# Performance work log

Hardware: AMD Instinct MI355X
Metric: run time of the kernel (lower is better)

Reference implementation:

```python
import jax, jax.numpy as jnp
import numpy as np

B, C, H, W = 8, 64, 256, 256
M1, M2 = 16, 16  # half of n_modes=(32,32); rfft last dim keeps n_modes[-1]//2


def setup_inputs() -> dict:
    key = jax.random.key(0)
    ks = jax.random.split(key, 7)
    scale = 1.0 / (C * C)
    return {
        "x": jax.random.normal(ks[0], (B, C, H, W), dtype=jnp.float32),
        "w1r": scale * jax.random.normal(ks[1], (C, C, M1, M2), dtype=jnp.float32),
        "w1i": scale * jax.random.normal(ks[2], (C, C, M1, M2), dtype=jnp.float32),
        "w2r": scale * jax.random.normal(ks[3], (C, C, M1, M2), dtype=jnp.float32),
        "w2i": scale * jax.random.normal(ks[4], (C, C, M1, M2), dtype=jnp.float32),
        "conv_w": jax.random.normal(ks[5], (C, C), dtype=jnp.float32) / np.sqrt(C),
        "conv_b": jax.random.normal(ks[6], (C,), dtype=jnp.float32) * 0.01,
    }


def reference(x, w1r, w1i, w2r, w2i, conv_w, conv_b):
    # ---- SpectralConv branch ----
    # rfft2 over spatial dims with 'ortho' norm: [b, c, H, W//2+1] complex
    x_ft = jnp.fft.rfftn(x, axes=(2, 3), norm="ortho")
    w1 = w1r + 1j * w1i  # positive-frequency corner weights [i, o, m1, m2]
    w2 = w2r + 1j * w2i  # negative-frequency corner weights
    top = jnp.einsum("bixy,ioxy->boxy", x_ft[:, :, :M1, :M2], w1)
    bot = jnp.einsum("bixy,ioxy->boxy", x_ft[:, :, -M1:, :M2], w2)
    out_ft = jnp.zeros((B, C, H, W // 2 + 1), dtype=x_ft.dtype)
    out_ft = out_ft.at[:, :, :M1, :M2].set(top)
    out_ft = out_ft.at[:, :, -M1:, :M2].set(bot)
    x1 = jnp.fft.irfftn(out_ft, s=(H, W), axes=(2, 3), norm="ortho")
    # ---- 1x1 Conv1d residual branch (channel mixing) ----
    x2 = jnp.einsum("oi,bixy->boxy", conv_w, x) + conv_b[None, :, None, None]
    return x1 + x2
```

## Files before the change

### kernel.cpp

```cpp
#include <hip/hip_runtime.h>
#include <math.h>


#define TWOPI_256 0.024543692606170259f
#define INV256    0.00390625f

#define NX   262144
#define NWT  2097152
#define NZ   2097152
#define O_TA  0
#define O_TB  4096
#define O_XR  20480
#define O_XI  (O_XR + NX)
#define O_WTR (O_XI + NX)
#define O_WTI (O_WTR + NWT)
#define O_YR  (O_WTI + NWT)
#define O_YI  (O_YR + NX)
#define O_ZR  (O_YI + NX)
#define O_ZI  (O_ZR + NZ)
#define O_TT  (O_ZI + NZ)
#define O_TD  (O_TT + 4096)

using s16x8 = __attribute__((ext_vector_type(8))) short;
using f32x4 = __attribute__((ext_vector_type(4))) float;

__device__ __forceinline__ unsigned short f2bf(float f) {
    union { float f; unsigned u; } a; a.f = f;
    unsigned r = (a.u + 0x7fffu + ((a.u >> 16) & 1u)) >> 16;
    return (unsigned short)r;
}

__global__ __launch_bounds__(256) void ktabs(unsigned short* __restrict__ tA,
                                             unsigned short* __restrict__ tB,
                                             unsigned short* __restrict__ tD) {
    int idx = blockIdx.x * 256 + threadIdx.x;
    if (idx < 8192) {
        int col = idx >> 8, w = idx & 255;
        int ky = col & 15;
        int mm = (ky * w) & 255;
        float s, c; sincosf((float)mm * TWOPI_256, &s, &c);
        tA[idx] = f2bf(col < 16 ? c * INV256 : -s * INV256);
    } else if (idx < 40960) {
        int j = idx - 8192;
        int kx2 = j >> 9, k = j & 511, h = k >> 1, p = k & 1;
        int kxi = kx2 & 31;
        int kx = (kxi < 16) ? kxi : (224 + kxi);
        int mm = (kx * h) & 255;
        float s, c; sincosf((float)mm * TWOPI_256, &s, &c);
        float v;
        if (kx2 < 32) v = p ? s : c;
        else          v = p ? c : -s;
        tB[j] = f2bf(v);
    } else {
        int j = idx - 40960;
        int ri = j >> 14, rem = j & 16383;
        int h = rem >> 6, k = rem & 63, kxi = k >> 1, p = k & 1;
        int kx = (kxi < 16) ? kxi : (224 + kxi);
        int mm = (kx * h) & 255;
        float s, c; sincosf((float)mm * TWOPI_256, &s, &c);
        float v;
        if (ri == 0) v = p ? -s : c;
        else         v = p ? c : s;
        tD[j] = f2bf(v);
    }
}

__global__ __launch_bounds__(256) void kab_fwd(const float* __restrict__ x,
                                               const unsigned short* __restrict__ tA,
                                               const unsigned short* __restrict__ tB,
                                               float* __restrict__ Xr,
                                               float* __restrict__ Xi) {
    __shared__ __align__(16) unsigned short xt[16384];
    __shared__ __align__(16) unsigned int   ub[4096];
    const int tid  = threadIdx.x;
    const int bc   = blockIdx.x;
    const int m    = tid & 15;
    const int g    = (tid >> 4) & 3;
    const int wave = tid >> 6;

    const float* xp = x + (size_t)bc * 65536;

    f32x4 acc[2][4];
#pragma unroll
    for (int a = 0; a < 2; ++a)
#pragma unroll
        for (int fn = 0; fn < 4; ++fn)
#pragma unroll
            for (int r = 0; r < 4; ++r) acc[a][fn][r] = 0.f;

    for (int ch = 0; ch < 4; ++ch) {
#pragma unroll
        for (int it = 0; it < 16; ++it) {
            int h  = it * 16 + (tid >> 4);
            int w4 = tid & 15;
            float4 v = *reinterpret_cast<const float4*>(xp + h * 256 + ch * 64 + w4 * 4);
            unsigned lo = (unsigned)f2bf(v.x) | ((unsigned)f2bf(v.y) << 16);
            unsigned hi = (unsigned)f2bf(v.z) | ((unsigned)f2bf(v.w) << 16);
            int wl  = w4 * 4;
            int blk = (wl >> 3) ^ (h & 7);
            char* p = reinterpret_cast<char*>(xt) + (h << 7) + (blk << 4) + ((wl & 7) << 1);
            *reinterpret_cast<uint2*>(p) = make_uint2(lo, hi);
        }
        __syncthreads();
#pragma unroll
        for (int ks = 0; ks < 2; ++ks) {
            s16x8 a0 = *reinterpret_cast<const s16x8*>(tA + m * 256        + ch * 64 + ks * 32 + 8 * g);
            s16x8 a1 = *reinterpret_cast<const s16x8*>(tA + (16 + m) * 256 + ch * 64 + ks * 32 + 8 * g);
#pragma unroll
            for (int fn = 0; fn < 4; ++fn) {
                int h   = wave * 64 + fn * 16 + m;
                int blk = (4 * ks + g) ^ (h & 7);
                s16x8 bf = *reinterpret_cast<const s16x8*>(
                    reinterpret_cast<const char*>(xt) + (h << 7) + (blk << 4));
                acc[0][fn] = __builtin_amdgcn_mfma_f32_16x16x32_bf16(a0, bf, acc[0][fn], 0, 0, 0);
                acc[1][fn] = __builtin_amdgcn_mfma_f32_16x16x32_bf16(a1, bf, acc[1][fn], 0, 0, 0);
            }
        }
        __syncthreads();
    }

#pragma unroll
    for (int fn = 0; fn < 4; ++fn) {
        int h = wave * 64 + fn * 16 + m;
#pragma unroll
        for (int r = 0; r < 4; ++r) {
            int ky = 4 * g + r;
            unsigned pk = (unsigned)f2bf(acc[0][fn][r]) | ((unsigned)f2bf(acc[1][fn][r]) << 16);
            int blk = (h >> 2) ^ (ky & 7);
            ub[ky * 256 + blk * 4 + (h & 3)] = pk;
        }
    }
    __syncthreads();

    f32x4 acc2;
#pragma unroll
    for (int r = 0; r < 4; ++r) acc2[r] = 0.f;
#pragma unroll
    for (int ks = 0; ks < 16; ++ks) {
        s16x8 a2 = *reinterpret_cast<const s16x8*>(tB + (wave * 16 + m) * 512 + ks * 32 + 8 * g);
        int blk = (4 * ks + g) ^ (m & 7);
        s16x8 b2 = *reinterpret_cast<const s16x8*>(
            reinterpret_cast<const char*>(ub) + m * 1024 + (blk << 4));
        acc2 = __builtin_amdgcn_mfma_f32_16x16x32_bf16(a2, b2, acc2, 0, 0, 0);
    }
#pragma unroll
    for (int r = 0; r < 4; ++r) {
        int kx2 = wave * 16 + 4 * g + r;
        if (kx2 < 32) Xr[(size_t)bc * 512 + kx2 * 16 + m]        = acc2[r];
        else          Xi[(size_t)bc * 512 + (kx2 - 32) * 16 + m] = acc2[r];
    }
}

__global__ __launch_bounds__(256) void kw_prep(const float* __restrict__ w1r,
                                               const float* __restrict__ w1i,
                                               const float* __restrict__ w2r,
                                               const float* __restrict__ w2i,
                                               float* __restrict__ Wtr,
                                               float* __restrict__ Wti) {
    __shared__ float lds[128][65];
    const int tid = threadIdx.x;
    const int a = blockIdx.x >> 6;
    const int i = blockIdx.x & 63;
    const float* src = (a == 0) ? w1r : (a == 1) ? w1i : (a == 2) ? w2r : w2i;
    float* dst = (a & 1) ? Wti : Wtr;
    const int kxoff = (a >> 1) << 4;
    const float* sp = src + (size_t)i * 16384;

    for (int p = 0; p < 2; ++p) {
        if (p) __syncthreads();
#pragma unroll
        for (int it = 0; it < 8; ++it) {
            int f4 = it * 256 + tid;
            int o = f4 >> 5, j4 = f4 & 31;
            float4 v = *reinterpret_cast<const float4*>(sp + o * 256 + p * 128 + j4 * 4);
            lds[j4 * 4 + 0][o] = v.x; lds[j4 * 4 + 1][o] = v.y;
            lds[j4 * 4 + 2][o] = v.z; lds[j4 * 4 + 3][o] = v.w;
        }
        __syncthreads();
        const int o = tid & 63, mq = tid >> 6;
#pragma unroll
        for (int r = 0; r < 32; ++r) {
            int lm = r * 4 + mq;
            int mky = p * 128 + lm;
            int mm = mky >> 4, ky = mky & 15;
            dst[((((size_t)(kxoff + mm)) * 16 + ky) * 64 + i) * 64 + o] = lds[lm][o];
        }
    }
}

__global__ __launch_bounds__(256) void ktrig(unsigned short* __restrict__ ttab) {
    int idx = blockIdx.x * 256 + threadIdx.x;
    int w = idx >> 5, kk = idx & 31, ky = kk >> 1;
    int mm = (ky * w) & 255;
    float s, c;
    sincosf((float)mm * TWOPI_256, &s, &c);
    ttab[idx] = f2bf((kk & 1) ? -s : c);
}

__global__ __launch_bounds__(256) void kc_mix(const float* __restrict__ Xr,
                                              const float* __restrict__ Xi,
                                              const float* __restrict__ Wtr,
                                              const float* __restrict__ Wti,
                                              float* __restrict__ Yr,
                                              float* __restrict__ Yi) {
    __shared__ float xsr[512], xsi[512];
    const int tid = threadIdx.x;
    const int mode = blockIdx.x;
#pragma unroll
    for (int r = 0; r < 2; ++r) {
        int bi = r * 256 + tid;
        xsr[bi] = Xr[(size_t)bi * 512 + mode];
        xsi[bi] = Xi[(size_t)bi * 512 + mode];
    }
    __syncthreads();
    const int o = tid & 63, bg = tid >> 6;
    float yr0 = 0.f, yi0 = 0.f, yr1 = 0.f, yi1 = 0.f;
    const float* wrp = Wtr + (size_t)mode * 4096;
    const float* wip = Wti + (size_t)mode * 4096;
#pragma unroll 8
    for (int i = 0; i < 64; ++i) {
        float wr = wrp[i * 64 + o], wi = wip[i * 64 + o];
        float xr = xsr[bg * 64 + i],        xi = xsi[bg * 64 + i];
        yr0 += xr * wr - xi * wi;  yi0 += xr * wi + xi * wr;
        float xr2 = xsr[(bg + 4) * 64 + i], xi2 = xsi[(bg + 4) * 64 + i];
        yr1 += xr2 * wr - xi2 * wi;  yi1 += xr2 * wi + xi2 * wr;
    }
    const int kxi = mode >> 4, kym = mode & 15;
    const size_t e0 = ((size_t)bg * 64 + o) * 512 + kym * 32 + kxi;
    const size_t e1 = ((size_t)(bg + 4) * 64 + o) * 512 + kym * 32 + kxi;
    Yr[e0] = yr0;  Yi[e0] = yi0;
    Yr[e1] = yr1;  Yi[e1] = yi1;
}

__global__ __launch_bounds__(256) void kd_mfma(const float* __restrict__ Yr2,
                                               const float* __restrict__ Yi2,
                                               const unsigned short* __restrict__ tD,
                                               float* __restrict__ Zr,
                                               float* __restrict__ Zi) {
    __shared__ __align__(16) unsigned short at[4096];
    __shared__ __align__(16) float zt[4][64][68];
    const int tid = threadIdx.x;
    const int bid = blockIdx.x;
    const int b  = bid >> 5;
    const int og = (bid >> 1) & 15;
    const int ri = bid & 1;

    {
        const int row = tid >> 2, q = tid & 3;
        const int ol = row >> 4, ky = row & 15;
        const float sc = (ky == 0) ? INV256 : 2.f * INV256;
        const size_t yb = ((size_t)(b * 64 + og * 4 + ol)) * 512 + ky * 32 + q * 8;
        f32x4 r0 = *reinterpret_cast<const f32x4*>(Yr2 + yb);
        f32x4 r1 = *reinterpret_cast<const f32x4*>(Yr2 + yb + 4);
        f32x4 i0 = *reinterpret_cast<const f32x4*>(Yi2 + yb);
        f32x4 i1 = *reinterpret_cast<const f32x4*>(Yi2 + yb + 4);
        unsigned wbuf[8];
#pragma unroll
        for (int t = 0; t < 4; ++t) {
            wbuf[t]     = (unsigned)f2bf(r0[t] * sc) | ((unsigned)f2bf(i0[t] * sc) << 16);
            wbuf[4 + t] = (unsigned)f2bf(r1[t] * sc) | ((unsigned)f2bf(i1[t] * sc) << 16);
        }
        char* base = reinterpret_cast<char*>(at) + row * 128;
        *reinterpret_cast<uint4*>(base + (((2 * q)     ^ (row & 7)) << 4)) = *reinterpret_cast<uint4*>(&wbuf[0]);
        *reinterpret_cast<uint4*>(base + (((2 * q + 1) ^ (row & 7)) << 4)) = *reinterpret_cast<uint4*>(&wbuf[4]);
    }
    __syncthreads();

    const int m = tid & 15, g = (tid >> 4) & 3, wid = tid >> 6;
    const int h0 = wid * 64;
    const unsigned short* td = tD + ri * 16384;

    f32x4 acc[4][4];
#pragma unroll
    for (int mf = 0; mf < 4; ++mf)
#pragma unroll
        for (int f = 0; f < 4; ++f)
#pragma unroll
            for (int r = 0; r < 4; ++r) acc[mf][f][r] = 0.f;

#pragma unroll
    for (int ks = 0; ks < 2; ++ks) {
        s16x8 af[4];
#pragma unroll
        for (int mf = 0; mf < 4; ++mf)
            af[mf] = *reinterpret_cast<const s16x8*>(
                reinterpret_cast<const char*>(at) + (mf * 16 + m) * 128
                + (((4 * ks + g) ^ (m & 7)) << 4));
#pragma unroll
        for (int f = 0; f < 4; ++f) {
            s16x8 bf = *reinterpret_cast<const s16x8*>(td + (h0 + f * 16 + m) * 64 + ks * 32 + 8 * g);
#pragma unroll
            for (int mf = 0; mf < 4; ++mf)
                acc[mf][f] = __builtin_amdgcn_mfma_f32_16x16x32_bf16(af[mf], bf, acc[mf][f], 0, 0, 0);
        }
    }

#pragma unroll
    for (int mf = 0; mf < 4; ++mf)
#pragma unroll
        for (int f = 0; f < 4; ++f)
#pragma unroll
            for (int r = 0; r < 4; ++r)
                zt[wid][f * 16 + m][mf * 16 + 4 * g + r] = acc[mf][f][r];
    __syncthreads();

    float* Zd = ri ? Zi : Zr;
    const int l = tid & 63;
    const int hloc = l >> 2, kg = l & 3;
#pragma unroll
    for (int ol = 0; ol < 4; ++ol)
#pragma unroll
        for (int hq = 0; hq < 4; ++hq) {
            f32x4 v = *reinterpret_cast<const f32x4*>(&zt[wid][hq * 16 + hloc][ol * 16 + 4 * kg]);
            size_t off = (((size_t)(b * 64 + og * 4 + ol)) * 256 + h0 + hq * 16 + hloc) * 16 + 4 * kg;
            *reinterpret_cast<f32x4*>(Zd + off) = v;
        }
}

__global__ __launch_bounds__(512) void ke_mfma(const float* __restrict__ x,
                                               const float* __restrict__ Zr,
                                               const float* __restrict__ Zi,
                                               const float* __restrict__ cw,
                                               const float* __restrict__ bias,
                                               const unsigned short* __restrict__ ttab,
                                               float* __restrict__ out) {
    __shared__ unsigned int bsx[8192];
    const int tid = threadIdx.x;
    const int b = blockIdx.x >> 8;
    const int h = blockIdx.x & 255;

    const size_t xbase = ((size_t)b * 64) * 65536 + (size_t)h * 256;
    const int w0s = (tid & 63) * 4;
    float4 va[4], vb[4];
#pragma unroll
    for (int it = 0; it < 4; ++it) {
        int ip = it * 8 + (tid >> 6);
        va[it] = *reinterpret_cast<const float4*>(x + xbase + (size_t)(2 * ip) * 65536 + w0s);
        vb[it] = *reinterpret_cast<const float4*>(x + xbase + (size_t)(2 * ip + 1) * 65536 + w0s);
    }

    const int m = tid & 15;
    const int g = (tid >> 4) & 3;
    const int wave = tid >> 6;
    const int o0 = (wave >> 1) * 16;
    const int f0 = (wave & 1) * 8;
    const int o = o0 + m;

    s16x8 a0, a1, az;
    {
        f32x4 p  = *reinterpret_cast<const f32x4*>(cw + o * 64 + 8 * g);
        f32x4 q  = *reinterpret_cast<const f32x4*>(cw + o * 64 + 8 * g + 4);
        f32x4 p2 = *reinterpret_cast<const f32x4*>(cw + o * 64 + 32 + 8 * g);
        f32x4 q2 = *reinterpret_cast<const f32x4*>(cw + o * 64 + 32 + 8 * g + 4);
        size_t zoff = (((size_t)b * 64 + o) * 256 + h) * 16 + 4 * g;
        f32x4 zr = *reinterpret_cast<const f32x4*>(Zr + zoff);
        f32x4 zi = *reinterpret_cast<const f32x4*>(Zi + zoff);
#pragma unroll
        for (int t = 0; t < 4; ++t) {
            a0[t]     = (short)f2bf(p[t]);  a0[t + 4] = (short)f2bf(q[t]);
            a1[t]     = (short)f2bf(p2[t]); a1[t + 4] = (short)f2bf(q2[t]);
            az[2 * t]     = (short)f2bf(zr[t]);
            az[2 * t + 1] = (short)f2bf(zi[t]);
        }
    }
    s16x8 btr[8];
#pragma unroll
    for (int f = 0; f < 8; ++f) {
        int w = (f0 + f) * 16 + m;
        btr[f] = *reinterpret_cast<const s16x8*>(ttab + w * 32 + 8 * g);
    }
    f32x4 bv = *reinterpret_cast<const f32x4*>(bias + o0 + 4 * g);

#pragma unroll
    for (int it = 0; it < 4; ++it) {
        int ip = it * 8 + (tid >> 6);
        const float* pa = reinterpret_cast<const float*>(&va[it]);
        const float* pb = reinterpret_cast<const float*>(&vb[it]);
#pragma unroll
        for (int j = 0; j < 4; ++j) {
            int w = w0s + j;
            int c = (w ^ (w >> 3)) & 7;
            unsigned pk = (unsigned)f2bf(pa[j]) | ((unsigned)f2bf(pb[j]) << 16);
            bsx[(w << 5) + ((((ip >> 2) ^ c) << 2) | (ip & 3))] = pk;
        }
    }
    __syncthreads();

    f32x4 acc[8];
#pragma unroll
    for (int f = 0; f < 8; ++f)
#pragma unroll
        for (int r = 0; r < 4; ++r) acc[f][r] = 0.f;

#pragma unroll
    for (int f = 0; f < 8; ++f) {
        int w = (f0 + f) * 16 + m;
        int c = (w ^ (w >> 3)) & 7;
        const char* rb = reinterpret_cast<const char*>(bsx) + (w << 7);
        s16x8 bx0 = *reinterpret_cast<const s16x8*>(rb + ((g ^ c) << 4));
        s16x8 bx1 = *reinterpret_cast<const s16x8*>(rb + (((4 + g) ^ c) << 4));
        acc[f] = __builtin_amdgcn_mfma_f32_16x16x32_bf16(a0, bx0, acc[f], 0, 0, 0);
        acc[f] = __builtin_amdgcn_mfma_f32_16x16x32_bf16(a1, bx1, acc[f], 0, 0, 0);
        acc[f] = __builtin_amdgcn_mfma_f32_16x16x32_bf16(az, btr[f], acc[f], 0, 0, 0);
    }

    float* ob = out + ((size_t)b * 64 + o0 + 4 * g) * 65536 + (size_t)h * 256;
#pragma unroll
    for (int f = 0; f < 8; ++f) {
        int wb = (f0 + f) * 16 + m;
#pragma unroll
        for (int r = 0; r < 4; ++r)
            ob[(size_t)r * 65536 + wb] = acc[f][r] + bv[r];
    }
}

extern "C" void kernel_launch(void* const* d_in, const int* in_sizes, int n_in,
                              void* d_out, int out_size, void* d_ws, size_t ws_size,
                              hipStream_t stream) {
    const float* x   = (const float*)d_in[0];
    const float* w1r = (const float*)d_in[1];
    const float* w1i = (const float*)d_in[2];
    const float* w2r = (const float*)d_in[3];
    const float* w2i = (const float*)d_in[4];
    const float* cw  = (const float*)d_in[5];
    const float* cb  = (const float*)d_in[6];
    float* out = (float*)d_out;
    float* ws  = (float*)d_ws;
    unsigned short* tA   = (unsigned short*)(ws + O_TA);
    unsigned short* tB   = (unsigned short*)(ws + O_TB);
    unsigned short* ttab = (unsigned short*)(ws + O_TT);
    unsigned short* tD   = (unsigned short*)(ws + O_TD);

    ktabs<<<288, 256, 0, stream>>>(tA, tB, tD);
    ktrig<<<32, 256, 0, stream>>>(ttab);
    kw_prep<<<256, 256, 0, stream>>>(w1r, w1i, w2r, w2i, ws + O_WTR, ws + O_WTI);
    kab_fwd<<<512, 256, 0, stream>>>(x, tA, tB, ws + O_XR, ws + O_XI);
    kc_mix<<<512, 256, 0, stream>>>(ws + O_XR, ws + O_XI, ws + O_WTR, ws + O_WTI,
                                    ws + O_YR, ws + O_YI);
    kd_mfma<<<256, 256, 0, stream>>>(ws + O_YR, ws + O_YI, tD, ws + O_ZR, ws + O_ZI);
    ke_mfma<<<2048, 512, 0, stream>>>(x, ws + O_ZR, ws + O_ZI, cw, cb, ttab, out);
}
```

Before: 147.3 us.

## Prefetch x chunks in forward DFT and split inverse kernels into finer blocks

kab_fwd now double-buffers the next 64-column chunk of x in registers while converting the current one, and hints a two-block occupancy target. kd_mfma is split four ways over h, giving each wave one 16-row tile and a smaller shared buffer, and launches four times more blocks. ke_mfma splits each row into two 128-wide halves with 256-thread blocks, halving shared memory per block and doubling the grid. The aim is to hide global-load latency and raise occupancy and parallelism. In exchange, each kd block now recomputes the shared Y tile, and the register-resident prefetch raises register pressure in kab_fwd.

```diff
diff --git a/kernel.cpp b/kernel.cpp
--- a/kernel.cpp
+++ b/kernel.cpp
@@ -65,11 +65,11 @@
     }
 }
 
-__global__ __launch_bounds__(256) void kab_fwd(const float* __restrict__ x,
-                                               const unsigned short* __restrict__ tA,
-                                               const unsigned short* __restrict__ tB,
-                                               float* __restrict__ Xr,
-                                               float* __restrict__ Xi) {
+__global__ __launch_bounds__(256, 2) void kab_fwd(const float* __restrict__ x,
+                                                  const unsigned short* __restrict__ tA,
+                                                  const unsigned short* __restrict__ tB,
+                                                  float* __restrict__ Xr,
+                                                  float* __restrict__ Xi) {
     __shared__ __align__(16) unsigned short xt[16384];
     __shared__ __align__(16) unsigned int   ub[4096];
     const int tid  = threadIdx.x;
@@ -79,6 +79,8 @@
     const int wave = tid >> 6;
 
     const float* xp = x + (size_t)bc * 65536;
+    const int hh = tid >> 4;
+    const int w4 = tid & 15;
 
     f32x4 acc[2][4];
 #pragma unroll
@@ -88,12 +90,24 @@
 #pragma unroll
             for (int r = 0; r < 4; ++r) acc[a][fn][r] = 0.f;
 
+    float4 stg[2][16];
+#pragma unroll
+    for (int it = 0; it < 16; ++it)
+        stg[0][it] = *reinterpret_cast<const float4*>(xp + (it * 16 + hh) * 256 + w4 * 4);
+
+#pragma unroll
     for (int ch = 0; ch < 4; ++ch) {
+        const int cur = ch & 1;
+        if (ch < 3) {
+#pragma unroll
+            for (int it = 0; it < 16; ++it)
+                stg[cur ^ 1][it] = *reinterpret_cast<const float4*>(
+                    xp + (it * 16 + hh) * 256 + (ch + 1) * 64 + w4 * 4);
+        }
 #pragma unroll
         for (int it = 0; it < 16; ++it) {
-            int h  = it * 16 + (tid >> 4);
-            int w4 = tid & 15;
-            float4 v = *reinterpret_cast<const float4*>(xp + h * 256 + ch * 64 + w4 * 4);
+            int h = it * 16 + hh;
+            float4 v = stg[cur][it];
             unsigned lo = (unsigned)f2bf(v.x) | ((unsigned)f2bf(v.y) << 16);
             unsigned hi = (unsigned)f2bf(v.z) | ((unsigned)f2bf(v.w) << 16);
             int wl  = w4 * 4;
@@ -238,12 +252,13 @@
                                                float* __restrict__ Zr,
                                                float* __restrict__ Zi) {
     __shared__ __align__(16) unsigned short at[4096];
-    __shared__ __align__(16) float zt[4][64][68];
+    __shared__ __align__(16) float zt[64][68];
     const int tid = threadIdx.x;
     const int bid = blockIdx.x;
-    const int b  = bid >> 5;
-    const int og = (bid >> 1) & 15;
-    const int ri = bid & 1;
+    const int b  = bid >> 7;
+    const int og = (bid >> 3) & 15;
+    const int ri = (bid >> 2) & 1;
+    const int hs = bid & 3;
 
     {
         const int row = tid >> 2, q = tid & 3;
@@ -267,84 +282,73 @@
     __syncthreads();
 
     const int m = tid & 15, g = (tid >> 4) & 3, wid = tid >> 6;
-    const int h0 = wid * 64;
     const unsigned short* td = tD + ri * 16384;
-
-    f32x4 acc[4][4];
+    const int hg = hs * 64 + wid * 16 + m;
+
+    f32x4 acc[4];
 #pragma unroll
     for (int mf = 0; mf < 4; ++mf)
 #pragma unroll
-        for (int f = 0; f < 4; ++f)
-#pragma unroll
-            for (int r = 0; r < 4; ++r) acc[mf][f][r] = 0.f;
+        for (int r = 0; r < 4; ++r) acc[mf][r] = 0.f;
 
 #pragma unroll
     for (int ks = 0; ks < 2; ++ks) {
-        s16x8 af[4];
-#pragma unroll
-        for (int mf = 0; mf < 4; ++mf)
-            af[mf] = *reinterpret_cast<const s16x8*>(
+        s16x8 bf = *reinterpret_cast<const s16x8*>(td + hg * 64 + ks * 32 + 8 * g);
+#pragma unroll
+        for (int mf = 0; mf < 4; ++mf) {
+            s16x8 af = *reinterpret_cast<const s16x8*>(
                 reinterpret_cast<const char*>(at) + (mf * 16 + m) * 128
                 + (((4 * ks + g) ^ (m & 7)) << 4));
-#pragma unroll
-        for (int f = 0; f < 4; ++f) {
-            s16x8 bf = *reinterpret_cast<const s16x8*>(td + (h0 + f * 16 + m) * 64 + ks * 32 + 8 * g);
-#pragma unroll
-            for (int mf = 0; mf < 4; ++mf)
-                acc[mf][f] = __builtin_amdgcn_mfma_f32_16x16x32_bf16(af[mf], bf, acc[mf][f], 0, 0, 0);
+            acc[mf] = __builtin_amdgcn_mfma_f32_16x16x32_bf16(af, bf, acc[mf], 0, 0, 0);
         }
     }
 
 #pragma unroll
     for (int mf = 0; mf < 4; ++mf)
 #pragma unroll
-        for (int f = 0; f < 4; ++f)
-#pragma unroll
-            for (int r = 0; r < 4; ++r)
-                zt[wid][f * 16 + m][mf * 16 + 4 * g + r] = acc[mf][f][r];
+        for (int r = 0; r < 4; ++r)
+            zt[wid * 16 + m][mf * 16 + 4 * g + r] = acc[mf][r];
     __syncthreads();
 
     float* Zd = ri ? Zi : Zr;
-    const int l = tid & 63;
-    const int hloc = l >> 2, kg = l & 3;
-#pragma unroll
-    for (int ol = 0; ol < 4; ++ol)
-#pragma unroll
-        for (int hq = 0; hq < 4; ++hq) {
-            f32x4 v = *reinterpret_cast<const f32x4*>(&zt[wid][hq * 16 + hloc][ol * 16 + 4 * kg]);
-            size_t off = (((size_t)(b * 64 + og * 4 + ol)) * 256 + h0 + hq * 16 + hloc) * 16 + 4 * kg;
-            *reinterpret_cast<f32x4*>(Zd + off) = v;
-        }
-}
-
-__global__ __launch_bounds__(512) void ke_mfma(const float* __restrict__ x,
+    const int ol = tid >> 6, hloc = (tid >> 2) & 15, kg = tid & 3;
+#pragma unroll
+    for (int hq = 0; hq < 4; ++hq) {
+        f32x4 v = *reinterpret_cast<const f32x4*>(&zt[hq * 16 + hloc][ol * 16 + 4 * kg]);
+        size_t off = (((size_t)(b * 64 + og * 4 + ol)) * 256 + hs * 64 + hq * 16 + hloc) * 16 + 4 * kg;
+        *reinterpret_cast<f32x4*>(Zd + off) = v;
+    }
+}
+
+__global__ __launch_bounds__(256) void ke_mfma(const float* __restrict__ x,
                                                const float* __restrict__ Zr,
                                                const float* __restrict__ Zi,
                                                const float* __restrict__ cw,
                                                const float* __restrict__ bias,
                                                const unsigned short* __restrict__ ttab,
                                                float* __restrict__ out) {
-    __shared__ unsigned int bsx[8192];
+    __shared__ unsigned int bsx[4096];
     const int tid = threadIdx.x;
-    const int b = blockIdx.x >> 8;
-    const int h = blockIdx.x & 255;
-
-    const size_t xbase = ((size_t)b * 64) * 65536 + (size_t)h * 256;
-    const int w0s = (tid & 63) * 4;
+    const int b  = blockIdx.x >> 9;
+    const int h  = (blockIdx.x >> 1) & 255;
+    const int wh = blockIdx.x & 1;
+    const int wbase = wh * 128;
+
+    const size_t xbase = ((size_t)b * 64) * 65536 + (size_t)h * 256 + wbase;
+    const int wl4 = (tid & 31) * 4;
+    const int ipg = tid >> 5;
     float4 va[4], vb[4];
 #pragma unroll
     for (int it = 0; it < 4; ++it) {
-        int ip = it * 8 + (tid >> 6);
-        va[it] = *reinterpret_cast<const float4*>(x + xbase + (size_t)(2 * ip) * 65536 + w0s);
-        vb[it] = *reinterpret_cast<const float4*>(x + xbase + (size_t)(2 * ip + 1) * 65536 + w0s);
+        int ip = it * 8 + ipg;
+        va[it] = *reinterpret_cast<const float4*>(x + xbase + (size_t)(2 * ip) * 65536 + wl4);
+        vb[it] = *reinterpret_cast<const float4*>(x + xbase + (size_t)(2 * ip + 1) * 65536 + wl4);
     }
 
     const int m = tid & 15;
     const int g = (tid >> 4) & 3;
     const int wave = tid >> 6;
-    const int o0 = (wave >> 1) * 16;
-    const int f0 = (wave & 1) * 8;
-    const int o = o0 + m;
+    const int o = wave * 16 + m;
 
     s16x8 a0, a1, az;
     {
@@ -366,22 +370,22 @@
     s16x8 btr[8];
 #pragma unroll
     for (int f = 0; f < 8; ++f) {
-        int w = (f0 + f) * 16 + m;
+        int w = wbase + f * 16 + m;
         btr[f] = *reinterpret_cast<const s16x8*>(ttab + w * 32 + 8 * g);
     }
-    f32x4 bv = *reinterpret_cast<const f32x4*>(bias + o0 + 4 * g);
+    f32x4 bv = *reinterpret_cast<const f32x4*>(bias + wave * 16 + 4 * g);
 
 #pragma unroll
     for (int it = 0; it < 4; ++it) {
-        int ip = it * 8 + (tid >> 6);
+        int ip = it * 8 + ipg;
         const float* pa = reinterpret_cast<const float*>(&va[it]);
         const float* pb = reinterpret_cast<const float*>(&vb[it]);
 #pragma unroll
         for (int j = 0; j < 4; ++j) {
-            int w = w0s + j;
-            int c = (w ^ (w >> 3)) & 7;
+            int wl = wl4 + j;
+            int c = (wl ^ (wl >> 3)) & 7;
             unsigned pk = (unsigned)f2bf(pa[j]) | ((unsigned)f2bf(pb[j]) << 16);
-            bsx[(w << 5) + ((((ip >> 2) ^ c) << 2) | (ip & 3))] = pk;
+            bsx[(wl << 5) + ((((ip >> 2) ^ c) << 2) | (ip & 3))] = pk;
         }
     }
     __syncthreads();
@@ -394,9 +398,9 @@
 
 #pragma unroll
     for (int f = 0; f < 8; ++f) {
-        int w = (f0 + f) * 16 + m;
-        int c = (w ^ (w >> 3)) & 7;
-        const char* rb = reinterpret_cast<const char*>(bsx) + (w << 7);
+        int wl = f * 16 + m;
+        int c = (wl ^ (wl >> 3)) & 7;
+        const char* rb = reinterpret_cast<const char*>(bsx) + (wl << 7);
         s16x8 bx0 = *reinterpret_cast<const s16x8*>(rb + ((g ^ c) << 4));
         s16x8 bx1 = *reinterpret_cast<const s16x8*>(rb + (((4 + g) ^ c) << 4));
         acc[f] = __builtin_amdgcn_mfma_f32_16x16x32_bf16(a0, bx0, acc[f], 0, 0, 0);
@@ -404,13 +408,12 @@
         acc[f] = __builtin_amdgcn_mfma_f32_16x16x32_bf16(az, btr[f], acc[f], 0, 0, 0);
     }
 
-    float* ob = out + ((size_t)b * 64 + o0 + 4 * g) * 65536 + (size_t)h * 256;
+    float* ob = out + ((size_t)(b * 64 + wave * 16 + 4 * g)) * 65536 + (size_t)h * 256 + wbase;
 #pragma unroll
     for (int f = 0; f < 8; ++f) {
-        int wb = (f0 + f) * 16 + m;
 #pragma unroll
         for (int r = 0; r < 4; ++r)
-            ob[(size_t)r * 65536 + wb] = acc[f][r] + bv[r];
+            ob[(size_t)r * 65536 + f * 16 + m] = acc[f][r] + bv[r];
     }
 }
 
@@ -437,6 +440,6 @@
     kab_fwd<<<512, 256, 0, stream>>>(x, tA, tB, ws + O_XR, ws + O_XI);
     kc_mix<<<512, 256, 0, stream>>>(ws + O_XR, ws + O_XI, ws + O_WTR, ws + O_WTI,
                                     ws + O_YR, ws + O_YI);
-    kd_mfma<<<256, 256, 0, stream>>>(ws + O_YR, ws + O_YI, tD, ws + O_ZR, ws + O_ZI);
-    ke_mfma<<<2048, 512, 0, stream>>>(x, ws + O_ZR, ws + O_ZI, cw, cb, ttab, out);
-}
+    kd_mfma<<<1024, 256, 0, stream>>>(ws + O_YR, ws + O_YI, tD, ws + O_ZR, ws + O_ZI);
+    ke_mfma<<<4096, 256, 0, stream>>>(x, ws + O_ZR, ws + O_ZI, cw, cb, ttab, out);
+}
```

Result: faster. 133.1 us (-9.6%).
